# Performance work log

Hardware: AMD Instinct MI355X
Metric: run time of the kernel (lower is better)

## Reference

```python
import jax, jax.numpy as jnp
import numpy as np

B, S, D, H, DFF = 2, 2048, 1024, 16, 4096
DH = D // H
EPS = 1e-8


def _alibi_bias(num_heads, seq_len, dtype=jnp.float32):
    # ALiBi slopes for power-of-two head counts: 2^(-8*(h+1)/H)
    h = jnp.arange(1, num_heads + 1, dtype=dtype)
    slopes = jnp.exp2(-8.0 * h / num_heads)          # [H]
    pos = jnp.arange(seq_len, dtype=dtype)
    rel = jnp.abs(pos[None, :] - pos[:, None])       # [S, S] |i-j|
    return -slopes[:, None, None] * rel[None]        # [H, S, S]


def _rmsnorm(x, scale):
    rms = jax.lax.rsqrt(jnp.mean(x * x, axis=-1, keepdims=True) + EPS)
    return scale * x * rms


def setup_inputs() -> dict:
    key = jax.random.key(0)
    ks = jax.random.split(key, 12)
    sd = 0.02
    return {
        "x": jax.random.normal(ks[0], (B, S, D), jnp.float32),
        "scale1": jnp.ones((D,), jnp.float32),
        "scale2": jnp.ones((D,), jnp.float32),
        "w_qkv": jax.random.normal(ks[1], (D, 3 * D), jnp.float32) * sd,
        "b_qkv": jnp.zeros((3 * D,), jnp.float32),
        "w_out": jax.random.normal(ks[2], (D, D), jnp.float32) * sd,
        "b_out": jnp.zeros((D,), jnp.float32),
        "w1": jax.random.normal(ks[3], (D, DFF), jnp.float32) * sd,
        "b1": jnp.zeros((DFF,), jnp.float32),
        "w2": jax.random.normal(ks[4], (DFF, D), jnp.float32) * sd,
        "b2": jnp.zeros((D,), jnp.float32),
    }


def reference(x, scale1, scale2, w_qkv, b_qkv, w_out, b_out, w1, b1, w2, b2):
    residual = x
    xn = _rmsnorm(x, scale1)
    qkv = xn @ w_qkv + b_qkv                                  # [B,S,3D]
    q, k, v = jnp.split(qkv, 3, axis=-1)
    def heads(t):
        return t.reshape(B, S, H, DH).transpose(0, 2, 1, 3)   # [B,H,S,DH]
    q, k, v = heads(q), heads(k), heads(v)
    scores = jnp.einsum("bhsd,bhtd->bhst", q, k) / (DH ** 0.5)
    scores = scores + _alibi_bias(H, S, scores.dtype)[None]
    attn = jax.nn.softmax(scores, axis=-1)
    out = jnp.einsum("bhst,bhtd->bhsd", attn, v)              # [B,H,S,DH]
    out = out.transpose(0, 2, 1, 3).reshape(B, S, D)
    x = residual + (out @ w_out + b_out)
    residual = x
    xn = _rmsnorm(x, scale2)
    h = jax.nn.gelu(xn @ w1 + b1, approximate=False)
    return residual + (h @ w2 + b2)
```

## Files before the change

kernel.cpp:

```cpp
#include <hip/hip_runtime.h>
#include <hip/hip_bf16.h>
#include <math.h>

#define B_ 2
#define S_ 2048
#define D_ 1024
#define H_ 16
#define DH_ 64
#define DFF_ 4096
#define M_ (B_*S_)

typedef __bf16 bf16;
typedef __bf16 bf16x8 __attribute__((ext_vector_type(8)));
typedef __bf16 bf16x4 __attribute__((ext_vector_type(4)));
typedef float f32x4 __attribute__((ext_vector_type(4)));

__device__ __forceinline__ void gll16(const void* g, void* l) {
  __builtin_amdgcn_global_load_lds(
      (const __attribute__((address_space(1))) void*)g,
      (__attribute__((address_space(3))) void*)l, 16, 0, 0);
}

__global__ __launch_bounds__(256) void rmsnorm_kernel(const float* __restrict__ x,
    const float* __restrict__ scale, bf16* __restrict__ out) {
  __shared__ float red[4];
  int row = blockIdx.x, t = threadIdx.x;
  const float4* xr = (const float4*)(x + (size_t)row * D_);
  float4 v = xr[t];
  float ss = v.x*v.x + v.y*v.y + v.z*v.z + v.w*v.w;
  #pragma unroll
  for (int off = 32; off > 0; off >>= 1) ss += __shfl_down(ss, off, 64);
  if ((t & 63) == 0) red[t >> 6] = ss;
  __syncthreads();
  float tot = red[0] + red[1] + red[2] + red[3];
  float r = rsqrtf(tot * (1.0f / D_) + 1e-8f);
  float4 sc = ((const float4*)scale)[t];
  bf16x4 o;
  o[0] = (bf16)(v.x * sc.x * r);
  o[1] = (bf16)(v.y * sc.y * r);
  o[2] = (bf16)(v.z * sc.z * r);
  o[3] = (bf16)(v.w * sc.w * r);
  *(bf16x4*)(out + (size_t)row * D_ + t * 4) = o;
}

__global__ __launch_bounds__(256) void reduce_rms_kernel(
    const bf16* __restrict__ p0, const bf16* __restrict__ p1,
    const float* __restrict__ x, const float* __restrict__ bias,
    const float* __restrict__ scale, float* __restrict__ x2, bf16* __restrict__ xn2) {
  __shared__ float red[4];
  int row = blockIdx.x, t = threadIdx.x;
  float4 xv = ((const float4*)(x + (size_t)row * D_))[t];
  float4 bv = ((const float4*)bias)[t];
  bf16x4 a = *(const bf16x4*)(p0 + (size_t)row * D_ + t * 4);
  bf16x4 b = *(const bf16x4*)(p1 + (size_t)row * D_ + t * 4);
  float s0 = xv.x + bv.x + (float)a[0] + (float)b[0];
  float s1 = xv.y + bv.y + (float)a[1] + (float)b[1];
  float s2 = xv.z + bv.z + (float)a[2] + (float)b[2];
  float s3 = xv.w + bv.w + (float)a[3] + (float)b[3];
  float4 o; o.x = s0; o.y = s1; o.z = s2; o.w = s3;
  ((float4*)(x2 + (size_t)row * D_))[t] = o;
  float ss = s0*s0 + s1*s1 + s2*s2 + s3*s3;
  #pragma unroll
  for (int off = 32; off > 0; off >>= 1) ss += __shfl_down(ss, off, 64);
  if ((t & 63) == 0) red[t >> 6] = ss;
  __syncthreads();
  float tot = red[0] + red[1] + red[2] + red[3];
  float r = rsqrtf(tot * (1.0f / D_) + 1e-8f);
  float4 sc = ((const float4*)scale)[t];
  bf16x4 on;
  on[0] = (bf16)(s0 * sc.x * r);
  on[1] = (bf16)(s1 * sc.y * r);
  on[2] = (bf16)(s2 * sc.z * r);
  on[3] = (bf16)(s3 * sc.w * r);
  *(bf16x4*)(xn2 + (size_t)row * D_ + t * 4) = on;
}

__global__ __launch_bounds__(256) void reduce_out_kernel(
    const bf16* __restrict__ p0, const bf16* __restrict__ p1,
    const float* __restrict__ x2, const float* __restrict__ bias,
    float* __restrict__ dout) {
  int row = blockIdx.x, t = threadIdx.x;
  float4 xv = ((const float4*)(x2 + (size_t)row * D_))[t];
  float4 bv = ((const float4*)bias)[t];
  bf16x4 a = *(const bf16x4*)(p0 + (size_t)row * D_ + t * 4);
  bf16x4 b = *(const bf16x4*)(p1 + (size_t)row * D_ + t * 4);
  float4 o;
  o.x = xv.x + bv.x + (float)a[0] + (float)b[0];
  o.y = xv.y + bv.y + (float)a[1] + (float)b[1];
  o.z = xv.z + bv.z + (float)a[2] + (float)b[2];
  o.w = xv.w + bv.w + (float)a[3] + (float)b[3];
  ((float4*)(dout + (size_t)row * D_))[t] = o;
}

__global__ __launch_bounds__(256) void wtrans_kernel(const float* __restrict__ W,
    bf16* __restrict__ Wt, int K, int N) {
  __shared__ float tile[32][33];
  int n0 = blockIdx.x * 32, k0 = blockIdx.y * 32;
  int tx = threadIdx.x & 31, ty = threadIdx.x >> 5;
  #pragma unroll
  for (int i = 0; i < 4; i++)
    tile[ty + i*8][tx] = W[(size_t)(k0 + ty + i*8) * N + n0 + tx];
  __syncthreads();
  #pragma unroll
  for (int i = 0; i < 4; i++)
    Wt[(size_t)(n0 + ty + i*8) * K + k0 + tx] = (bf16)tile[tx][ty + i*8];
}

__global__ __launch_bounds__(256) void vtrans_kernel(const bf16* __restrict__ Vin,
    bf16* __restrict__ Vt) {
  __shared__ bf16 tile[32][34];
  size_t base = (size_t)blockIdx.z * (S_ * DH_);
  int s0 = blockIdx.x * 32, d0 = blockIdx.y * 32;
  int tx = threadIdx.x & 31, ty = threadIdx.x >> 5;
  #pragma unroll
  for (int i = 0; i < 4; i++)
    tile[ty + i*8][tx] = Vin[base + (size_t)(s0 + ty + i*8) * DH_ + d0 + tx];
  __syncthreads();
  #pragma unroll
  for (int i = 0; i < 4; i++)
    Vt[base + (size_t)(d0 + ty + i*8) * S_ + s0 + tx] = tile[tx][ty + i*8];
}

__device__ __forceinline__ float gelu_fast(float x) {
  float e = __builtin_amdgcn_exp2f(2.3022585093f * x * (1.0f + 0.044715f * x * x));
  return x * e / (1.0f + e);
}

template<int MODE>
__global__ __launch_bounds__(256) void gemm_kernel(
    const bf16* __restrict__ A, const bf16* __restrict__ Bt,
    const float* __restrict__ bias, void* __restrict__ outp, void* __restrict__ outp2,
    int M, int N, int K, int lda) {
  __shared__ __align__(16) bf16 As[2][128 * 32];
  __shared__ __align__(16) bf16 Bs[2][128 * 32];
  int t = threadIdx.x;
  int wave = t >> 6, lane = t & 63;
  int lm = lane & 15, lg = lane >> 4;
  int m0 = blockIdx.y * 128, n0 = blockIdx.x * 128;
  size_t koff = (size_t)blockIdx.z * K;
  int wm = (wave >> 1) * 64, wn = (wave & 1) * 64;
  f32x4 acc[4][4] = {};

  int srow = t >> 2, sslot = t & 3;
  int scol = (sslot ^ ((srow >> 1) & 3)) * 8;
  const bf16* Ag = A + (size_t)(m0 + srow) * lda + koff + scol;
  const bf16* Bg = Bt + (size_t)(n0 + srow) * lda + koff + scol;
  size_t half = (size_t)64 * lda;

  int rsw = (lm >> 1) & 3;

  gll16(Ag, As[0] + t * 8);
  gll16(Ag + half, As[0] + 2048 + t * 8);
  gll16(Bg, Bs[0] + t * 8);
  gll16(Bg + half, Bs[0] + 2048 + t * 8);

  int buf = 0;
  for (int k0 = 0; k0 < K; k0 += 32, buf ^= 1) {
    __syncthreads();
    if (k0 + 32 < K) {
      gll16(Ag + k0 + 32, As[buf ^ 1] + t * 8);
      gll16(Ag + k0 + 32 + half, As[buf ^ 1] + 2048 + t * 8);
      gll16(Bg + k0 + 32, Bs[buf ^ 1] + t * 8);
      gll16(Bg + k0 + 32 + half, Bs[buf ^ 1] + 2048 + t * 8);
    }
    const bf16* Ab = As[buf];
    const bf16* Bb = Bs[buf];
    bf16x8 af[4], bfr[4];
    #pragma unroll
    for (int i = 0; i < 4; i++)
      af[i] = *(const bf16x8*)(Ab + (wm + i * 16 + lm) * 32 + (lg ^ rsw) * 8);
    #pragma unroll
    for (int j = 0; j < 4; j++)
      bfr[j] = *(const bf16x8*)(Bb + (wn + j * 16 + lm) * 32 + (lg ^ rsw) * 8);
    #pragma unroll
    for (int i = 0; i < 4; i++)
      #pragma unroll
      for (int j = 0; j < 4; j++)
        acc[i][j] = __builtin_amdgcn_mfma_f32_16x16x32_bf16(af[i], bfr[j], acc[i][j], 0, 0, 0);
  }

  bf16* pout = (MODE == 5) ? ((blockIdx.z == 0) ? (bf16*)outp : (bf16*)outp2) : (bf16*)outp;

  #pragma unroll
  for (int i = 0; i < 4; i++) {
    int row = m0 + wm + i * 16 + lg * 4;
    #pragma unroll
    for (int j = 0; j < 4; j++) {
      int col = n0 + wn + j * 16 + lm;
      float bcol = (MODE == 5) ? 0.f : bias[col];
      #pragma unroll
      for (int r = 0; r < 4; r++) {
        float v = acc[i][j][r] + bcol;
        int rr = row + r;
        if (MODE == 0) {
          int which = col >> 10, d = col & 1023;
          int hh = d >> 6, dh = d & 63;
          int bb = rr >> 11, s = rr & 2047;
          ((bf16*)outp)[(size_t)which * ((size_t)B_*H_*S_*DH_) +
              ((size_t)(bb * H_ + hh) * S_ + s) * DH_ + dh] = (bf16)v;
        } else if (MODE == 2) {
          ((bf16*)outp)[(size_t)rr * N + col] = (bf16)gelu_fast(v);
        } else {
          pout[(size_t)rr * N + col] = (bf16)v;
        }
      }
    }
  }
}

#define PSTR 68
__global__ __launch_bounds__(256, 3) void attn_kernel(
    const bf16* __restrict__ q, const bf16* __restrict__ k,
    const bf16* __restrict__ vT, bf16* __restrict__ ao) {
  __shared__ __align__(16) bf16 Ks[2][64 * 64];
  __shared__ __align__(16) bf16 Vs[2][64 * 64];
  __shared__ __align__(16) bf16 Ps[4 * 16 * PSTR];
  int t = threadIdx.x, wave = t >> 6, lane = t & 63;
  int lm = lane & 15, lg = lane >> 4;
  int q0 = blockIdx.x * 64;
  int h = blockIdx.y, b = blockIdx.z;
  size_t base = (size_t)(b * H_ + h) * ((size_t)S_ * DH_);
  const bf16* Q = q + base;
  const bf16* K = k + base;
  const bf16* V = vT + base;
  const float LOG2E = 1.4426950408889634f;
  float sl2 = exp2f(-0.5f * (float)(h + 1)) * LOG2E;
  float nslope = -sl2;
  const float qscale = 0.125f * LOG2E;
  const float FMAX = 8.0f;

  int W = (int)(24.0f / sl2);
  int jlo = (q0 - W) >> 6; if (jlo < 0) jlo = 0;
  int jhi = ((q0 + 63 + W) >> 6) + 1; if (jhi > S_ / 64) jhi = S_ / 64;

  bf16x8 qf[2];
  #pragma unroll
  for (int h2 = 0; h2 < 2; h2++) {
    bf16x8 v = *(const bf16x8*)(Q + (size_t)(q0 + wave * 16 + lm) * DH_ + h2 * 32 + lg * 8);
    #pragma unroll
    for (int e = 0; e < 8; e++) v[e] = (bf16)((float)v[e] * qscale);
    qf[h2] = v;
  }

  int row0 = t >> 3, jslot = t & 7;
  int gsw = (jslot ^ (row0 & 7)) << 3;
  const bf16* Ksrc0 = K + (size_t)row0 * DH_ + gsw;
  const bf16* Vsrc0 = V + (size_t)row0 * S_ + gsw;

  {
    int jt = jlo << 6;
    gll16(Ksrc0 + (size_t)jt * DH_, Ks[0] + (size_t)t * 8);
    gll16(Ksrc0 + (size_t)(jt + 32) * DH_, Ks[0] + (size_t)(t + 256) * 8);
    gll16(Vsrc0 + jt, Vs[0] + (size_t)t * 8);
    gll16(Vsrc0 + (size_t)32 * S_ + jt, Vs[0] + (size_t)(t + 256) * 8);
  }

  f32x4 oacc[4] = {};
  float rs[4] = {0.f, 0.f, 0.f, 0.f};
  int psw = lm & 7;

  for (int jj = jlo; jj < jhi; ++jj) {
    int buf = (jj - jlo) & 1;
    int jt = jj << 6;
    __syncthreads();
    if (jj + 1 < jhi) {
      int jn = (jj + 1) << 6;
      gll16(Ksrc0 + (size_t)jn * DH_, Ks[buf ^ 1] + (size_t)t * 8);
      gll16(Ksrc0 + (size_t)(jn + 32) * DH_, Ks[buf ^ 1] + (size_t)(t + 256) * 8);
      gll16(Vsrc0 + jn, Vs[buf ^ 1] + (size_t)t * 8);
      gll16(Vsrc0 + (size_t)32 * S_ + jn, Vs[buf ^ 1] + (size_t)(t + 256) * 8);
    }
    const bf16* Kb = Ks[buf];
    const bf16* Vb = Vs[buf];

    f32x4 sc[4];
    #pragma unroll
    for (int tt = 0; tt < 4; tt++) {
      f32x4 a = {-FMAX, -FMAX, -FMAX, -FMAX};
      int krow = tt * 16 + lm;
      bf16x8 kb0 = *(const bf16x8*)(Kb + (size_t)(krow * 8 + (lg ^ psw)) * 8);
      bf16x8 kb1 = *(const bf16x8*)(Kb + (size_t)(krow * 8 + ((lg + 4) ^ psw)) * 8);
      a = __builtin_amdgcn_mfma_f32_16x16x32_bf16(qf[0], kb0, a, 0, 0, 0);
      a = __builtin_amdgcn_mfma_f32_16x16x32_bf16(qf[1], kb1, a, 0, 0, 0);
      sc[tt] = a;
    }

    bf16* Pw = Ps + wave * (16 * PSTR);
    int i0 = q0 + wave * 16 + lg * 4;
    #pragma unroll
    for (int tt = 0; tt < 4; tt++) {
      float f0 = (float)(i0 - jt - tt * 16 - lm);
      #pragma unroll
      for (int r = 0; r < 4; r++) {
        float s2 = fmaf(nslope, fabsf(f0 + (float)r), sc[tt][r]);
        float p = __builtin_amdgcn_exp2f(s2);
        rs[r] += p;
        Pw[(lg * 4 + r) * PSTR + tt * 16 + lm] = (bf16)p;
      }
    }

    bf16x8 ap0 = *(const bf16x8*)(Pw + lm * PSTR + lg * 8);
    bf16x8 ap1 = *(const bf16x8*)(Pw + lm * PSTR + 32 + lg * 8);
    #pragma unroll
    for (int tt = 0; tt < 4; tt++) {
      int vrow = tt * 16 + lm;
      bf16x8 vb0 = *(const bf16x8*)(Vb + (size_t)(vrow * 8 + (lg ^ psw)) * 8);
      bf16x8 vb1 = *(const bf16x8*)(Vb + (size_t)(vrow * 8 + ((lg + 4) ^ psw)) * 8);
      oacc[tt] = __builtin_amdgcn_mfma_f32_16x16x32_bf16(ap0, vb0, oacc[tt], 0, 0, 0);
      oacc[tt] = __builtin_amdgcn_mfma_f32_16x16x32_bf16(ap1, vb1, oacc[tt], 0, 0, 0);
    }
  }

  #pragma unroll
  for (int r = 0; r < 4; r++) {
    #pragma unroll
    for (int off = 1; off < 16; off <<= 1)
      rs[r] += __shfl_xor(rs[r], off, 16);
  }

  #pragma unroll
  for (int r = 0; r < 4; r++) {
    float inv = 1.0f / rs[r];
    int row = q0 + wave * 16 + lg * 4 + r;
    #pragma unroll
    for (int tt = 0; tt < 4; tt++) {
      int col = h * 64 + tt * 16 + lm;
      ao[((size_t)(b * S_) + row) * D_ + col] = (bf16)(oacc[tt][r] * inv);
    }
  }
}

extern "C" void kernel_launch(void* const* d_in, const int* in_sizes, int n_in,
                              void* d_out, int out_size, void* d_ws, size_t ws_size,
                              hipStream_t stream) {
  const float* x      = (const float*)d_in[0];
  const float* scale1 = (const float*)d_in[1];
  const float* scale2 = (const float*)d_in[2];
  const float* w_qkv  = (const float*)d_in[3];
  const float* b_qkv  = (const float*)d_in[4];
  const float* w_out  = (const float*)d_in[5];
  const float* b_out  = (const float*)d_in[6];
  const float* w1     = (const float*)d_in[7];
  const float* b1     = (const float*)d_in[8];
  const float* w2     = (const float*)d_in[9];
  const float* b2     = (const float*)d_in[10];

  char* ws = (char*)d_ws;
  const size_t MB = 1024 * 1024;
  bf16* xn    = (bf16*)(ws + 0);
  bf16* qb    = (bf16*)(ws + 8*MB);
  bf16* kb    = (bf16*)(ws + 16*MB);
  bf16* vb    = (bf16*)(ws + 24*MB);
  bf16* vT    = (bf16*)(ws + 32*MB);
  bf16* wqkvT = (bf16*)(ws + 40*MB);
  bf16* woutT = (bf16*)(ws + 46*MB);
  bf16* w1T   = (bf16*)(ws + 48*MB);
  bf16* w2T   = (bf16*)(ws + 56*MB);
  float* x2   = (float*)(ws + 64*MB);
  bf16* xn2   = qb;
  bf16* pp0   = kb;
  bf16* pp1   = vb;
  bf16* hbuf  = kb;
  bf16* qp0   = xn;
  bf16* qp1   = w1T;
  bf16* ao    = xn;

  dim3 blk(256);
  wtrans_kernel<<<dim3(3072/32, 1024/32), blk, 0, stream>>>(w_qkv, wqkvT, 1024, 3072);
  wtrans_kernel<<<dim3(1024/32, 1024/32), blk, 0, stream>>>(w_out, woutT, 1024, 1024);
  wtrans_kernel<<<dim3(4096/32, 1024/32), blk, 0, stream>>>(w1, w1T, 1024, 4096);
  wtrans_kernel<<<dim3(1024/32, 4096/32), blk, 0, stream>>>(w2, w2T, 4096, 1024);

  rmsnorm_kernel<<<dim3(M_), blk, 0, stream>>>(x, scale1, xn);

  gemm_kernel<0><<<dim3(3072/128, M_/128, 1), blk, 0, stream>>>(
      xn, wqkvT, b_qkv, qb, nullptr, M_, 3072, 1024, 1024);

  vtrans_kernel<<<dim3(S_/32, DH_/32, B_*H_), blk, 0, stream>>>(vb, vT);

  attn_kernel<<<dim3(S_/64, H_, B_), blk, 0, stream>>>(qb, kb, vT, ao);

  gemm_kernel<5><<<dim3(1024/128, M_/128, 2), blk, 0, stream>>>(
      ao, woutT, nullptr, pp0, pp1, M_, 1024, 512, 1024);
  reduce_rms_kernel<<<dim3(M_), blk, 0, stream>>>(pp0, pp1, x, b_out, scale2, x2, xn2);

  gemm_kernel<2><<<dim3(4096/128, M_/128, 1), blk, 0, stream>>>(
      xn2, w1T, b1, hbuf, nullptr, M_, 4096, 1024, 1024);

  gemm_kernel<5><<<dim3(1024/128, M_/128, 2), blk, 0, stream>>>(
      hbuf, w2T, nullptr, qp0, qp1, M_, 1024, 2048, 4096);
  reduce_out_kernel<<<dim3(M_), blk, 0, stream>>>(qp0, qp1, x2, b2, (float*)d_out);
}
```

Before: 377.7 us.

## Triple-buffer GEMM LDS tiles with two-stage prefetch and partial vmcnt waits

Moves the GEMM main loop from double to triple buffering in LDS. Two K tiles are prefetched ahead, and each iteration uses an explicit s_waitcnt on vmcnt that leaves the newest four global-to-LDS loads in flight before the barrier. The aim is to hide global load latency behind MFMA work instead of draining every load each step. In exchange the kernel uses 50% more LDS, which can lower occupancy, and it depends on hand-coded waitcnt encodings being correct for the target.

New measurement: 373.6 us. About the same (-1.1%).

```diff
diff --git a/kernel.cpp b/kernel.cpp
--- a/kernel.cpp
+++ b/kernel.cpp
@@ -20,6 +20,9 @@
       (const __attribute__((address_space(1))) void*)g,
       (__attribute__((address_space(3))) void*)l, 16, 0, 0);
 }
+
+#define WAITCNT_VM4 0xF74
+#define WAITCNT_VM0 0xF70
 
 __global__ __launch_bounds__(256) void rmsnorm_kernel(const float* __restrict__ x,
     const float* __restrict__ scale, bf16* __restrict__ out) {
@@ -131,8 +134,8 @@
     const bf16* __restrict__ A, const bf16* __restrict__ Bt,
     const float* __restrict__ bias, void* __restrict__ outp, void* __restrict__ outp2,
     int M, int N, int K, int lda) {
-  __shared__ __align__(16) bf16 As[2][128 * 32];
-  __shared__ __align__(16) bf16 Bs[2][128 * 32];
+  __shared__ __align__(16) bf16 As[3][128 * 32];
+  __shared__ __align__(16) bf16 Bs[3][128 * 32];
   int t = threadIdx.x;
   int wave = t >> 6, lane = t & 63;
   int lm = lane & 15, lg = lane >> 4;
@@ -146,37 +149,50 @@
   const bf16* Ag = A + (size_t)(m0 + srow) * lda + koff + scol;
   const bf16* Bg = Bt + (size_t)(n0 + srow) * lda + koff + scol;
   size_t half = (size_t)64 * lda;
-
   int rsw = (lm >> 1) & 3;
+  int nk = K >> 5;
 
   gll16(Ag, As[0] + t * 8);
   gll16(Ag + half, As[0] + 2048 + t * 8);
   gll16(Bg, Bs[0] + t * 8);
   gll16(Bg + half, Bs[0] + 2048 + t * 8);
+  if (nk > 1) {
+    gll16(Ag + 32, As[1] + t * 8);
+    gll16(Ag + 32 + half, As[1] + 2048 + t * 8);
+    gll16(Bg + 32, Bs[1] + t * 8);
+    gll16(Bg + 32 + half, Bs[1] + 2048 + t * 8);
+  }
 
   int buf = 0;
-  for (int k0 = 0; k0 < K; k0 += 32, buf ^= 1) {
-    __syncthreads();
-    if (k0 + 32 < K) {
-      gll16(Ag + k0 + 32, As[buf ^ 1] + t * 8);
-      gll16(Ag + k0 + 32 + half, As[buf ^ 1] + 2048 + t * 8);
-      gll16(Bg + k0 + 32, Bs[buf ^ 1] + t * 8);
-      gll16(Bg + k0 + 32 + half, Bs[buf ^ 1] + 2048 + t * 8);
+  for (int j = 0; j < nk; ++j) {
+    if (j + 1 < nk) __builtin_amdgcn_s_waitcnt(WAITCNT_VM4);
+    else            __builtin_amdgcn_s_waitcnt(WAITCNT_VM0);
+    __builtin_amdgcn_s_barrier();
+    if (j + 2 < nk) {
+      int k2 = (j + 2) << 5;
+      int nbuf = buf + 2; if (nbuf >= 3) nbuf -= 3;
+      bf16* Ad = As[nbuf];
+      bf16* Bd = Bs[nbuf];
+      gll16(Ag + k2, Ad + t * 8);
+      gll16(Ag + k2 + half, Ad + 2048 + t * 8);
+      gll16(Bg + k2, Bd + t * 8);
+      gll16(Bg + k2 + half, Bd + 2048 + t * 8);
     }
     const bf16* Ab = As[buf];
     const bf16* Bb = Bs[buf];
+    if (++buf == 3) buf = 0;
     bf16x8 af[4], bfr[4];
     #pragma unroll
     for (int i = 0; i < 4; i++)
       af[i] = *(const bf16x8*)(Ab + (wm + i * 16 + lm) * 32 + (lg ^ rsw) * 8);
     #pragma unroll
-    for (int j = 0; j < 4; j++)
-      bfr[j] = *(const bf16x8*)(Bb + (wn + j * 16 + lm) * 32 + (lg ^ rsw) * 8);
+    for (int j2 = 0; j2 < 4; j2++)
+      bfr[j2] = *(const bf16x8*)(Bb + (wn + j2 * 16 + lm) * 32 + (lg ^ rsw) * 8);
     #pragma unroll
     for (int i = 0; i < 4; i++)
       #pragma unroll
-      for (int j = 0; j < 4; j++)
-        acc[i][j] = __builtin_amdgcn_mfma_f32_16x16x32_bf16(af[i], bfr[j], acc[i][j], 0, 0, 0);
+      for (int j2 = 0; j2 < 4; j2++)
+        acc[i][j2] = __builtin_amdgcn_mfma_f32_16x16x32_bf16(af[i], bfr[j2], acc[i][j2], 0, 0, 0);
   }
 
   bf16* pout = (MODE == 5) ? ((blockIdx.z == 0) ? (bf16*)outp : (bf16*)outp2) : (bf16*)outp;
```
